# Kernel optimization log

Measured on AMD Instinct MI355X. Metric: run time of the kernel, lower is better.

## Reference

```python
import jax, jax.numpy as jnp
import numpy as np
from jax import lax

B, CIN, COUT, H, W = 4, 256, 256, 64, 64
KH = KW = 3
K = KH * KW
GN_GROUPS = 32
EPS = 1e-5


def setup_inputs() -> dict:
    key = jax.random.key(0)
    ks = jax.random.split(key, 6)
    x = jax.random.normal(ks[0], (B, CIN, H, W), jnp.float32)
    # offset predictor conv: 3x3, 18 out channels, with bias (init small so offsets stay near 0)
    offset_w = jax.random.normal(ks[1], (2 * K, CIN, KH, KW), jnp.float32) * 0.01
    offset_b = jax.random.normal(ks[2], (2 * K,), jnp.float32) * 0.01
    # deformable conv weight (no bias), He-ish scale
    deform_w = jax.random.normal(ks[3], (COUT, CIN, KH, KW), jnp.float32) * (1.0 / np.sqrt(CIN * K))
    gn_gamma = jnp.ones((COUT,), jnp.float32)
    gn_beta = jnp.zeros((COUT,), jnp.float32)
    return {"x": x, "offset_w": offset_w, "offset_b": offset_b,
            "deform_w": deform_w, "gn_gamma": gn_gamma, "gn_beta": gn_beta}


def _deform_conv(x, offset, weight):
    """Deformable conv v1, stride=1, pad=1, dil=1, deformable_groups=1.
    x: [B,C,H,W]; offset: [B,2K,H,W] with (dy,dx) per kernel tap; weight: [O,C,3,3].
    """
    b, c, h, w = x.shape
    off = offset.reshape(b, K, 2, h, w)
    # base sampling grid per kernel tap: p = p0 - pad + k
    ky, kx = jnp.meshgrid(jnp.arange(KH), jnp.arange(KW), indexing="ij")
    base_y = (jnp.arange(h, dtype=jnp.float32) - 1.0)[None, :, None] + ky.reshape(K).astype(jnp.float32)[:, None, None]  # [K,H,1]
    base_x = (jnp.arange(w, dtype=jnp.float32) - 1.0)[None, None, :] + kx.reshape(K).astype(jnp.float32)[:, None, None]  # [K,1,W]
    py = base_y[None] + off[:, :, 0]  # [B,K,H,W]
    px = base_x[None] + off[:, :, 1]  # [B,K,H,W]

    y0 = jnp.floor(py)
    x0 = jnp.floor(px)
    ty = py - y0
    tx = px - x0
    y0 = y0.astype(jnp.int32)
    x0 = x0.astype(jnp.int32)

    x_hw = x.transpose(0, 2, 3, 1).reshape(b, h * w, c)  # [B,HW,C]

    def corner(yi, xi, wgt):
        valid = (yi >= 0) & (yi < h) & (xi >= 0) & (xi < w)
        yc = jnp.clip(yi, 0, h - 1)
        xc = jnp.clip(xi, 0, w - 1)
        idx = (yc * w + xc).reshape(b, K * h * w)
        v = jnp.take_along_axis(x_hw, idx[..., None], axis=1)  # [B,KHW,C]
        return v * (wgt * valid.astype(wgt.dtype)).reshape(b, K * h * w, 1)

    samp = (corner(y0, x0, (1 - ty) * (1 - tx))
            + corner(y0, x0 + 1, (1 - ty) * tx)
            + corner(y0 + 1, x0, ty * (1 - tx))
            + corner(y0 + 1, x0 + 1, ty * tx))  # [B,KHW,C]
    samp = samp.reshape(b, K, h, w, c)
    return jnp.einsum("bkhwc,ock->bohw", samp, weight.reshape(weight.shape[0], c, K))


def reference(x, offset_w, offset_b, deform_w, gn_gamma, gn_beta):
    # offset = conv3x3(x) + bias
    offset = lax.conv_general_dilated(
        x, offset_w, window_strides=(1, 1), padding=((1, 1), (1, 1)),
        dimension_numbers=("NCHW", "OIHW", "NCHW")) + offset_b[None, :, None, None]
    out = _deform_conv(x, offset, deform_w)
    # GroupNorm(32, COUT) + ReLU
    b, c, h, w = out.shape
    g = out.reshape(b, GN_GROUPS, (c // GN_GROUPS) * h * w)
    mu = g.mean(axis=2, keepdims=True)
    var = g.var(axis=2, keepdims=True)
    g = (g - mu) * lax.rsqrt(var + EPS)
    out = g.reshape(b, c, h, w) * gn_gamma[None, :, None, None] + gn_beta[None, :, None, None]
    return jax.nn.relu(out)
```

## Files before the change

kernel.cpp:

```cpp
#include <hip/hip_runtime.h>
#include <hip/hip_bf16.h>
#include <stdint.h>


typedef unsigned short u16;
typedef __bf16 bf16x8 __attribute__((ext_vector_type(8)));
typedef float f32x4_t __attribute__((ext_vector_type(4)));

#define HW 4096

__device__ __forceinline__ uint32_t f32_to_bf16_rne(float f) {
  uint32_t u = __builtin_bit_cast(uint32_t, f);
  return (u + 0x7FFFu + ((u >> 16) & 1u)) >> 16;
}
__device__ __forceinline__ float bf_lo(uint32_t u) {
  return __builtin_bit_cast(float, u << 16);
}
__device__ __forceinline__ float bf_hi(uint32_t u) {
  return __builtin_bit_cast(float, u & 0xFFFF0000u);
}
__device__ __forceinline__ uint32_t blend2(uint32_t a, uint32_t b, uint32_t c,
                                           uint32_t d, float4 mw) {
  float lo = mw.x * bf_lo(a) + mw.y * bf_lo(b) + mw.z * bf_lo(c) + mw.w * bf_lo(d);
  float hi = mw.x * bf_hi(a) + mw.y * bf_hi(b) + mw.z * bf_hi(c) + mw.w * bf_hi(d);
  return f32_to_bf16_rne(lo) | (f32_to_bf16_rne(hi) << 16);
}

__global__ __launch_bounds__(256) void k_transpose(const float* __restrict__ x,
                                                   u16* __restrict__ xt) {
  __shared__ float tile[32][33];
  int b = blockIdx.z;
  int c0 = blockIdx.y * 32;
  int p0 = blockIdx.x * 32;
  int tx = threadIdx.x, ty = threadIdx.y;
#pragma unroll
  for (int j = 0; j < 32; j += 8)
    tile[ty + j][tx] = x[(b * 256 + c0 + ty + j) * HW + p0 + tx];
  __syncthreads();
  int wid = ty * 32 + tx;
  int cp = wid & 15;
  int pr = wid >> 4;
#pragma unroll
  for (int j = 0; j < 2; j++) {
    int p = pr + j * 16;
    uint32_t lo = f32_to_bf16_rne(tile[cp * 2][p]);
    uint32_t hi = f32_to_bf16_rne(tile[cp * 2 + 1][p]);
    *(uint32_t*)&xt[(b * HW + p0 + p) * 256 + c0 + cp * 2] = lo | (hi << 16);
  }
}

__global__ __launch_bounds__(256) void k_prep(const float* __restrict__ wsrc,
                                              const float* __restrict__ ow,
                                              u16* __restrict__ warr,
                                              u16* __restrict__ owm,
                                              float* __restrict__ part) {
  int bid = blockIdx.x;
  if (bid < 2304) {
    int e = bid * 256 + threadIdx.x;
    int kk = e & 7, m = (e >> 3) & 255, g = (e >> 11) & 7, kc = e >> 14;
    int cin = (kc & 3) * 64 + g * 8 + kk;
    int tap = kc >> 2;
    warr[e] = (u16)f32_to_bf16_rne(wsrc[m * 2304 + cin * 9 + tap]);
  } else if (bid < 2592) {
    int e = (bid - 2304) * 256 + threadIdx.x;
    int kk = e & 7, m = (e >> 3) & 31, g = (e >> 8) & 7, kc = e >> 11;
    int cin = (kc & 3) * 64 + g * 8 + kk;
    int tap = kc >> 2;
    float v = (m < 18) ? ow[m * 2304 + cin * 9 + tap] : 0.f;
    owm[e] = (u16)f32_to_bf16_rne(v);
  } else {
    part[threadIdx.x] = 0.f;
  }
}

__global__ __launch_bounds__(512, 4) void k_conv(
    const u16* __restrict__ xt, const u16* __restrict__ warr,
    const u16* __restrict__ owm, const float* __restrict__ ob,
    float* __restrict__ out, float* __restrict__ part) {
  __shared__ char smem[54272];
  u16* stage = (u16*)smem;
  float* off_part = (float*)(smem + 33792);
  int4* ci_s = (int4*)smem;
  float4* mw_s = (float4*)(smem + 4608);
  u16* b_s = (u16*)(smem + 9216);

  int tid = threadIdx.x;
  int lane = tid & 63;
  int wm = tid >> 6;
  int b = blockIdx.x >> 7;
  int pt = blockIdx.x & 127;
  int p0 = pt * 32;
  int yrow = p0 >> 6, xbase = p0 & 63;

  {
    u16* st = stage + wm * 2112;
    int q = lane & 15, pq = lane >> 4;
    int oct = lane & 7, pxs = lane >> 3;
    f32x4_t a2[2][2] = {};
#pragma unroll 1
    for (int kc = wm; kc < 36; kc += 8) {
      int tap = kc >> 2, cc = kc & 3;
      int ky = tap / 3, kx = tap % 3;
      int yy = yrow + ky - 1;
      bool vy = (yy >= 0) && (yy < 64);
#pragma unroll
      for (int i = 0; i < 4; i++) {
        int px = i * 8 + pxs;
        int xx2 = xbase + px + kx - 1;
        uint4 v = make_uint4(0u, 0u, 0u, 0u);
        if (vy && xx2 >= 0 && xx2 < 64)
          v = *(const uint4*)&xt[(b * HW + yy * 64 + xx2) * 256 + cc * 64 + oct * 8];
        *(uint4*)&st[oct * 264 + px * 8] = v;
      }
#pragma unroll
      for (int ks = 0; ks < 2; ks++) {
        int g = ks * 4 + pq;
        const u16* ab = owm + kc * 2048 + g * 256;
#pragma unroll
        for (int s = 0; s < 2; s++) {
          bf16x8 bfr = *(bf16x8*)&st[g * 264 + (s * 16 + q) * 8];
#pragma unroll
          for (int im = 0; im < 2; im++) {
            bf16x8 af = *(const bf16x8*)&ab[(im * 16 + q) * 8];
            a2[s][im] = __builtin_amdgcn_mfma_f32_16x16x32_bf16(af, bfr, a2[s][im], 0, 0, 0);
          }
        }
      }
    }
#pragma unroll
    for (int s = 0; s < 2; s++)
#pragma unroll
      for (int im = 0; im < 2; im++)
#pragma unroll
        for (int r = 0; r < 4; r++) {
          int oc = im * 16 + pq * 4 + r;
          if (oc < 18) off_part[(wm * 32 + s * 16 + q) * 20 + oc] = a2[s][im][r];
        }
  }
  __syncthreads();
  for (int it = tid; it < 288; it += 512) {
    int tap = it >> 5;
    int px = it & 31;
    float dy = ob[2 * tap], dx = ob[2 * tap + 1];
#pragma unroll
    for (int wv = 0; wv < 8; wv++) {
      dy += off_part[(wv * 32 + px) * 20 + 2 * tap];
      dx += off_part[(wv * 32 + px) * 20 + 2 * tap + 1];
    }
    int ky = tap / 3, kx = tap % 3;
    int p = p0 + px;
    int yq = p >> 6, xq = p & 63;
    float py = (float)(yq - 1 + ky) + dy;
    float pxx = (float)(xq - 1 + kx) + dx;
    float y0f = floorf(py), x0f = floorf(pxx);
    float ty = py - y0f, tx = pxx - x0f;
    int y0 = (int)y0f, x0 = (int)x0f;
    int y1 = y0 + 1, x1 = x0 + 1;
    float wy0 = 1.f - ty, wy1 = ty, wx0 = 1.f - tx, wx1 = tx;
    bool vy0 = (y0 >= 0) && (y0 < 64), vy1 = (y1 >= 0) && (y1 < 64);
    bool vx0 = (x0 >= 0) && (x0 < 64), vx1 = (x1 >= 0) && (x1 < 64);
    int cy0 = min(max(y0, 0), 63), cy1 = min(max(y1, 0), 63);
    int cx0 = min(max(x0, 0), 63), cx1 = min(max(x1, 0), 63);
    int base = b * HW;
    int4 ci;
    ci.x = (base + cy0 * 64 + cx0) * 256;
    ci.y = (base + cy0 * 64 + cx1) * 256;
    ci.z = (base + cy1 * 64 + cx0) * 256;
    ci.w = (base + cy1 * 64 + cx1) * 256;
    float4 mw;
    mw.x = wy0 * wx0 * ((vy0 && vx0) ? 1.f : 0.f);
    mw.y = wy0 * wx1 * ((vy0 && vx1) ? 1.f : 0.f);
    mw.z = wy1 * wx0 * ((vy1 && vx0) ? 1.f : 0.f);
    mw.w = wy1 * wx1 * ((vy1 && vx1) ? 1.f : 0.f);
    ci_s[it] = ci;
    mw_s[it] = mw;
  }
  __syncthreads();

  {
    int oct8 = tid & 15;
    int pxg = tid >> 4;
    int sub = pxg >> 4;
    int pxw = pxg & 15;
    int col = lane & 15;
    int pq = lane >> 4;
    f32x4_t acc[2][2] = {};

    int4 ci = ci_s[pxg];
    float4 mw = mw_s[pxg];
    int e = oct8 * 8;
    uint4 c0 = *(const uint4*)&xt[ci.x + e];
    uint4 c1 = *(const uint4*)&xt[ci.y + e];
    uint4 c2 = *(const uint4*)&xt[ci.z + e];
    uint4 c3 = *(const uint4*)&xt[ci.w + e];

#pragma unroll 1
    for (int dccg = 0; dccg < 18; dccg++) {
      u16* bb = b_s + (dccg & 1) * 4352;
      uint4 u;
      u.x = blend2(c0.x, c1.x, c2.x, c3.x, mw);
      u.y = blend2(c0.y, c1.y, c2.y, c3.y, mw);
      u.z = blend2(c0.z, c1.z, c2.z, c3.z, mw);
      u.w = blend2(c0.w, c1.w, c2.w, c3.w, mw);
      *(uint4*)&bb[sub * 2176 + oct8 * 136 + pxw * 8] = u;
      __syncthreads();
      if (dccg < 17) {
        int nx = dccg + 1;
        int tapn = nx >> 1;
        int en = (nx & 1) * 128 + oct8 * 8;
        int4 cin = ci_s[tapn * 32 + pxg];
        float4 mwn = mw_s[tapn * 32 + pxg];
        c0 = *(const uint4*)&xt[cin.x + en];
        c1 = *(const uint4*)&xt[cin.y + en];
        c2 = *(const uint4*)&xt[cin.z + en];
        c3 = *(const uint4*)&xt[cin.w + en];
        mw = mwn;
      }
      int tap = dccg >> 1, dcc = dccg & 1;
#pragma unroll
      for (int ks = 0; ks < 4; ks++) {
        int ro = ks * 4 + pq;
        bf16x8 b0 = *(bf16x8*)&bb[ro * 136 + col * 8];
        bf16x8 b1 = *(bf16x8*)&bb[2176 + ro * 136 + col * 8];
        int kc = tap * 4 + dcc * 2 + (ks >> 1);
        int g = (ks & 1) * 4 + pq;
        const u16* ab = warr + kc * 16384 + g * 2048 + (wm * 32 + col) * 8;
#pragma unroll
        for (int im = 0; im < 2; im++) {
          bf16x8 af = *(const bf16x8*)&ab[im * 128];
          acc[0][im] = __builtin_amdgcn_mfma_f32_16x16x32_bf16(af, b0, acc[0][im], 0, 0, 0);
          acc[1][im] = __builtin_amdgcn_mfma_f32_16x16x32_bf16(af, b1, acc[1][im], 0, 0, 0);
        }
      }
    }

#pragma unroll
    for (int im = 0; im < 2; im++) {
      float s = 0.f, ss = 0.f;
#pragma unroll
      for (int sb = 0; sb < 2; sb++) {
        int n = p0 + sb * 16 + col;
#pragma unroll
        for (int r = 0; r < 4; r++) {
          int m = wm * 32 + im * 16 + pq * 4 + r;
          float v = acc[sb][im][r];
          out[(b * 256 + m) * HW + n] = v;
          s += v;
          ss += v * v;
        }
      }
#pragma unroll
      for (int msk = 1; msk <= 16; msk <<= 1) {
        s += __shfl_xor(s, msk);
        ss += __shfl_xor(ss, msk);
      }
      if ((lane & 31) == 0) {
        int g = wm * 4 + im * 2 + (lane >> 5);
        float* pp = part + (b * 32 + g) * 2;
        atomicAdd(pp, s);
        atomicAdd(pp + 1, ss);
      }
    }
  }
}

__global__ __launch_bounds__(256) void k_gn_apply(float* __restrict__ out,
                                                  const float2* __restrict__ part,
                                                  const float* __restrict__ gamma,
                                                  const float* __restrict__ beta) {
  __shared__ float sga, sbe;
  int gid = blockIdx.x * 256 + threadIdx.x;
  int c = (gid >> 10) & 255;
  int bb = gid >> 18;
  if (threadIdx.x == 0) {
    float2 p = part[bb * 32 + (c >> 3)];
    float mu = p.x / 32768.f;
    float var = p.y / 32768.f - mu * mu;
    float rs = rsqrtf(var + 1e-5f);
    float ga = gamma[c] * rs;
    sga = ga;
    sbe = beta[c] - mu * ga;
  }
  __syncthreads();
  float ga = sga, be = sbe;
  float4 v = ((const float4*)out)[gid];
  v.x = fmaxf(v.x * ga + be, 0.f);
  v.y = fmaxf(v.y * ga + be, 0.f);
  v.z = fmaxf(v.z * ga + be, 0.f);
  v.w = fmaxf(v.w * ga + be, 0.f);
  ((float4*)out)[gid] = v;
}

extern "C" void kernel_launch(void* const* d_in, const int* in_sizes, int n_in,
                              void* d_out, int out_size, void* d_ws, size_t ws_size,
                              hipStream_t stream) {
  const float* x = (const float*)d_in[0];
  const float* offset_w = (const float*)d_in[1];
  const float* offset_b = (const float*)d_in[2];
  const float* deform_w = (const float*)d_in[3];
  const float* gn_gamma = (const float*)d_in[4];
  const float* gn_beta = (const float*)d_in[5];
  float* out = (float*)d_out;
  char* ws = (char*)d_ws;

  u16* xt = (u16*)ws;
  u16* warr = (u16*)(ws + 8388608);
  u16* owm = (u16*)(ws + 9568256);
  float* part = (float*)(ws + 9715712);

  k_transpose<<<dim3(128, 8, 4), dim3(32, 8), 0, stream>>>(x, xt);
  k_prep<<<dim3(2593), dim3(256), 0, stream>>>(deform_w, offset_w, warr, owm, part);
  k_conv<<<dim3(512), dim3(512), 0, stream>>>(xt, warr, owm, offset_b, out, part);
  k_gn_apply<<<dim3(4096), dim3(256), 0, stream>>>(out, (const float2*)part, gn_gamma, gn_beta);
}
```

Measured before the change: 163.4 us.

## Double conv pixel tile to a full row and merge prep kernels

The deformable conv kernel now handles 64 pixels (one full image row) per block instead of 32. That halves the grid to 256 blocks and doubles the MFMA accumulators, so each weight fragment loaded from global memory is reused across twice as many pixels. The offset-prediction phase is split into two halves of 4 waves each, and the block index is swizzled across batch and rows. The transpose and weight-prep kernels are merged into one launch to save a kernel launch. The trade-off is higher register pressure and LDS use, since the occupancy hint was dropped, and fewer blocks on a 256-CU device.

```diff
diff --git a/kernel.cpp b/kernel.cpp
--- a/kernel.cpp
+++ b/kernel.cpp
@@ -26,54 +26,52 @@
   return f32_to_bf16_rne(lo) | (f32_to_bf16_rne(hi) << 16);
 }
 
-__global__ __launch_bounds__(256) void k_transpose(const float* __restrict__ x,
-                                                   u16* __restrict__ xt) {
+__global__ __launch_bounds__(256) void k_pre(const float* __restrict__ x,
+                                             const float* __restrict__ wsrc,
+                                             const float* __restrict__ ow,
+                                             u16* __restrict__ xt,
+                                             u16* __restrict__ warr,
+                                             u16* __restrict__ owm,
+                                             float* __restrict__ part) {
   __shared__ float tile[32][33];
-  int b = blockIdx.z;
-  int c0 = blockIdx.y * 32;
-  int p0 = blockIdx.x * 32;
-  int tx = threadIdx.x, ty = threadIdx.y;
-#pragma unroll
-  for (int j = 0; j < 32; j += 8)
-    tile[ty + j][tx] = x[(b * 256 + c0 + ty + j) * HW + p0 + tx];
-  __syncthreads();
-  int wid = ty * 32 + tx;
-  int cp = wid & 15;
-  int pr = wid >> 4;
-#pragma unroll
-  for (int j = 0; j < 2; j++) {
-    int p = pr + j * 16;
-    uint32_t lo = f32_to_bf16_rne(tile[cp * 2][p]);
-    uint32_t hi = f32_to_bf16_rne(tile[cp * 2 + 1][p]);
-    *(uint32_t*)&xt[(b * HW + p0 + p) * 256 + c0 + cp * 2] = lo | (hi << 16);
-  }
-}
-
-__global__ __launch_bounds__(256) void k_prep(const float* __restrict__ wsrc,
-                                              const float* __restrict__ ow,
-                                              u16* __restrict__ warr,
-                                              u16* __restrict__ owm,
-                                              float* __restrict__ part) {
   int bid = blockIdx.x;
-  if (bid < 2304) {
-    int e = bid * 256 + threadIdx.x;
+  int tid = threadIdx.x;
+  if (bid < 4096) {
+    int bx = bid & 127, by = (bid >> 7) & 7, bz = bid >> 10;
+    int c0 = by * 32, p0 = bx * 32;
+    int tx = tid & 31, ty = tid >> 5;
+#pragma unroll
+    for (int j = 0; j < 32; j += 8)
+      tile[ty + j][tx] = x[(bz * 256 + c0 + ty + j) * HW + p0 + tx];
+    __syncthreads();
+    int cp = tid & 15;
+    int pr = tid >> 4;
+#pragma unroll
+    for (int j = 0; j < 2; j++) {
+      int p = pr + j * 16;
+      uint32_t lo = f32_to_bf16_rne(tile[cp * 2][p]);
+      uint32_t hi = f32_to_bf16_rne(tile[cp * 2 + 1][p]);
+      *(uint32_t*)&xt[(bz * HW + p0 + p) * 256 + c0 + cp * 2] = lo | (hi << 16);
+    }
+  } else if (bid < 6400) {
+    int e = (bid - 4096) * 256 + tid;
     int kk = e & 7, m = (e >> 3) & 255, g = (e >> 11) & 7, kc = e >> 14;
     int cin = (kc & 3) * 64 + g * 8 + kk;
     int tap = kc >> 2;
     warr[e] = (u16)f32_to_bf16_rne(wsrc[m * 2304 + cin * 9 + tap]);
-  } else if (bid < 2592) {
-    int e = (bid - 2304) * 256 + threadIdx.x;
+  } else if (bid < 6688) {
+    int e = (bid - 6400) * 256 + tid;
     int kk = e & 7, m = (e >> 3) & 31, g = (e >> 8) & 7, kc = e >> 11;
     int cin = (kc & 3) * 64 + g * 8 + kk;
     int tap = kc >> 2;
     float v = (m < 18) ? ow[m * 2304 + cin * 9 + tap] : 0.f;
     owm[e] = (u16)f32_to_bf16_rne(v);
   } else {
-    part[threadIdx.x] = 0.f;
-  }
-}
-
-__global__ __launch_bounds__(512, 4) void k_conv(
+    part[tid] = 0.f;
+  }
+}
+
+__global__ __launch_bounds__(512) void k_conv(
     const u16* __restrict__ xt, const u16* __restrict__ warr,
     const u16* __restrict__ owm, const float* __restrict__ ob,
     float* __restrict__ out, float* __restrict__ part) {
@@ -81,32 +79,34 @@
   u16* stage = (u16*)smem;
   float* off_part = (float*)(smem + 33792);
   int4* ci_s = (int4*)smem;
-  float4* mw_s = (float4*)(smem + 4608);
-  u16* b_s = (u16*)(smem + 9216);
+  float4* mw_s = (float4*)(smem + 9216);
+  u16* b_s = (u16*)(smem + 18432);
 
   int tid = threadIdx.x;
   int lane = tid & 63;
   int wm = tid >> 6;
-  int b = blockIdx.x >> 7;
-  int pt = blockIdx.x & 127;
-  int p0 = pt * 32;
-  int yrow = p0 >> 6, xbase = p0 & 63;
+  int wk = (blockIdx.x & 7) * 32 + (blockIdx.x >> 3);
+  int b = wk >> 6;
+  int pt = wk & 63;
+  int p0 = pt * 64;
 
   {
     u16* st = stage + wm * 2112;
+    int half = wm >> 2, ww = wm & 3;
+    int xh = half * 32;
     int q = lane & 15, pq = lane >> 4;
     int oct = lane & 7, pxs = lane >> 3;
     f32x4_t a2[2][2] = {};
 #pragma unroll 1
-    for (int kc = wm; kc < 36; kc += 8) {
+    for (int kc = ww; kc < 36; kc += 4) {
       int tap = kc >> 2, cc = kc & 3;
       int ky = tap / 3, kx = tap % 3;
-      int yy = yrow + ky - 1;
+      int yy = pt + ky - 1;
       bool vy = (yy >= 0) && (yy < 64);
 #pragma unroll
       for (int i = 0; i < 4; i++) {
         int px = i * 8 + pxs;
-        int xx2 = xbase + px + kx - 1;
+        int xx2 = xh + px + kx - 1;
         uint4 v = make_uint4(0u, 0u, 0u, 0u);
         if (vy && xx2 >= 0 && xx2 < 64)
           v = *(const uint4*)&xt[(b * HW + yy * 64 + xx2) * 256 + cc * 64 + oct * 8];
@@ -138,20 +138,19 @@
         }
   }
   __syncthreads();
-  for (int it = tid; it < 288; it += 512) {
-    int tap = it >> 5;
-    int px = it & 31;
+  for (int it = tid; it < 576; it += 512) {
+    int tap = it >> 6;
+    int px = it & 63;
+    int half = px >> 5, px32 = px & 31;
     float dy = ob[2 * tap], dx = ob[2 * tap + 1];
 #pragma unroll
-    for (int wv = 0; wv < 8; wv++) {
-      dy += off_part[(wv * 32 + px) * 20 + 2 * tap];
-      dx += off_part[(wv * 32 + px) * 20 + 2 * tap + 1];
+    for (int wv = 0; wv < 4; wv++) {
+      dy += off_part[((half * 4 + wv) * 32 + px32) * 20 + 2 * tap];
+      dx += off_part[((half * 4 + wv) * 32 + px32) * 20 + 2 * tap + 1];
     }
     int ky = tap / 3, kx = tap % 3;
-    int p = p0 + px;
-    int yq = p >> 6, xq = p & 63;
-    float py = (float)(yq - 1 + ky) + dy;
-    float pxx = (float)(xq - 1 + kx) + dx;
+    float py = (float)(pt - 1 + ky) + dy;
+    float pxx = (float)(px - 1 + kx) + dx;
     float y0f = floorf(py), x0f = floorf(pxx);
     float ty = py - y0f, tx = pxx - x0f;
     int y0 = (int)y0f, x0 = (int)x0f;
@@ -180,41 +179,62 @@
   {
     int oct8 = tid & 15;
     int pxg = tid >> 4;
-    int sub = pxg >> 4;
+    int suba = pxg >> 4;
     int pxw = pxg & 15;
     int col = lane & 15;
     int pq = lane >> 4;
-    f32x4_t acc[2][2] = {};
-
-    int4 ci = ci_s[pxg];
-    float4 mw = mw_s[pxg];
-    int e = oct8 * 8;
-    uint4 c0 = *(const uint4*)&xt[ci.x + e];
-    uint4 c1 = *(const uint4*)&xt[ci.y + e];
-    uint4 c2 = *(const uint4*)&xt[ci.z + e];
-    uint4 c3 = *(const uint4*)&xt[ci.w + e];
+    f32x4_t acc[4][2] = {};
+
+    int e0 = oct8 * 8;
+    int4 cia = ci_s[pxg];
+    float4 mwa = mw_s[pxg];
+    int4 cib = ci_s[32 + pxg];
+    float4 mwb = mw_s[32 + pxg];
+    uint4 g0 = *(const uint4*)&xt[cia.x + e0];
+    uint4 g1 = *(const uint4*)&xt[cia.y + e0];
+    uint4 g2 = *(const uint4*)&xt[cia.z + e0];
+    uint4 g3 = *(const uint4*)&xt[cia.w + e0];
+    uint4 h0 = *(const uint4*)&xt[cib.x + e0];
+    uint4 h1 = *(const uint4*)&xt[cib.y + e0];
+    uint4 h2 = *(const uint4*)&xt[cib.z + e0];
+    uint4 h3 = *(const uint4*)&xt[cib.w + e0];
 
 #pragma unroll 1
     for (int dccg = 0; dccg < 18; dccg++) {
-      u16* bb = b_s + (dccg & 1) * 4352;
-      uint4 u;
-      u.x = blend2(c0.x, c1.x, c2.x, c3.x, mw);
-      u.y = blend2(c0.y, c1.y, c2.y, c3.y, mw);
-      u.z = blend2(c0.z, c1.z, c2.z, c3.z, mw);
-      u.w = blend2(c0.w, c1.w, c2.w, c3.w, mw);
-      *(uint4*)&bb[sub * 2176 + oct8 * 136 + pxw * 8] = u;
+      u16* bb = b_s + (dccg & 1) * 8704;
+      {
+        uint4 u;
+        u.x = blend2(g0.x, g1.x, g2.x, g3.x, mwa);
+        u.y = blend2(g0.y, g1.y, g2.y, g3.y, mwa);
+        u.z = blend2(g0.z, g1.z, g2.z, g3.z, mwa);
+        u.w = blend2(g0.w, g1.w, g2.w, g3.w, mwa);
+        *(uint4*)&bb[suba * 2176 + oct8 * 136 + pxw * 8] = u;
+      }
+      {
+        uint4 u;
+        u.x = blend2(h0.x, h1.x, h2.x, h3.x, mwb);
+        u.y = blend2(h0.y, h1.y, h2.y, h3.y, mwb);
+        u.z = blend2(h0.z, h1.z, h2.z, h3.z, mwb);
+        u.w = blend2(h0.w, h1.w, h2.w, h3.w, mwb);
+        *(uint4*)&bb[(suba + 2) * 2176 + oct8 * 136 + pxw * 8] = u;
+      }
       __syncthreads();
       if (dccg < 17) {
         int nx = dccg + 1;
         int tapn = nx >> 1;
-        int en = (nx & 1) * 128 + oct8 * 8;
-        int4 cin = ci_s[tapn * 32 + pxg];
-        float4 mwn = mw_s[tapn * 32 + pxg];
-        c0 = *(const uint4*)&xt[cin.x + en];
-        c1 = *(const uint4*)&xt[cin.y + en];
-        c2 = *(const uint4*)&xt[cin.z + en];
-        c3 = *(const uint4*)&xt[cin.w + en];
-        mw = mwn;
+        int en = (nx & 1) * 128 + e0;
+        cia = ci_s[tapn * 64 + pxg];
+        mwa = mw_s[tapn * 64 + pxg];
+        cib = ci_s[tapn * 64 + 32 + pxg];
+        mwb = mw_s[tapn * 64 + 32 + pxg];
+        g0 = *(const uint4*)&xt[cia.x + en];
+        g1 = *(const uint4*)&xt[cia.y + en];
+        g2 = *(const uint4*)&xt[cia.z + en];
+        g3 = *(const uint4*)&xt[cia.w + en];
+        h0 = *(const uint4*)&xt[cib.x + en];
+        h1 = *(const uint4*)&xt[cib.y + en];
+        h2 = *(const uint4*)&xt[cib.z + en];
+        h3 = *(const uint4*)&xt[cib.w + en];
       }
       int tap = dccg >> 1, dcc = dccg & 1;
 #pragma unroll
@@ -222,14 +242,18 @@
         int ro = ks * 4 + pq;
         bf16x8 b0 = *(bf16x8*)&bb[ro * 136 + col * 8];
         bf16x8 b1 = *(bf16x8*)&bb[2176 + ro * 136 + col * 8];
+        bf16x8 b2 = *(bf16x8*)&bb[4352 + ro * 136 + col * 8];
+        bf16x8 b3 = *(bf16x8*)&bb[6528 + ro * 136 + col * 8];
         int kc = tap * 4 + dcc * 2 + (ks >> 1);
-        int g = (ks & 1) * 4 + pq;
-        const u16* ab = warr + kc * 16384 + g * 2048 + (wm * 32 + col) * 8;
+        int gg = (ks & 1) * 4 + pq;
+        const u16* ab = warr + kc * 16384 + gg * 2048 + (wm * 32 + col) * 8;
 #pragma unroll
         for (int im = 0; im < 2; im++) {
           bf16x8 af = *(const bf16x8*)&ab[im * 128];
           acc[0][im] = __builtin_amdgcn_mfma_f32_16x16x32_bf16(af, b0, acc[0][im], 0, 0, 0);
           acc[1][im] = __builtin_amdgcn_mfma_f32_16x16x32_bf16(af, b1, acc[1][im], 0, 0, 0);
+          acc[2][im] = __builtin_amdgcn_mfma_f32_16x16x32_bf16(af, b2, acc[2][im], 0, 0, 0);
+          acc[3][im] = __builtin_amdgcn_mfma_f32_16x16x32_bf16(af, b3, acc[3][im], 0, 0, 0);
         }
       }
     }
@@ -238,7 +262,7 @@
     for (int im = 0; im < 2; im++) {
       float s = 0.f, ss = 0.f;
 #pragma unroll
-      for (int sb = 0; sb < 2; sb++) {
+      for (int sb = 0; sb < 4; sb++) {
         int n = p0 + sb * 16 + col;
 #pragma unroll
         for (int r = 0; r < 4; r++) {
@@ -255,8 +279,8 @@
         ss += __shfl_xor(ss, msk);
       }
       if ((lane & 31) == 0) {
-        int g = wm * 4 + im * 2 + (lane >> 5);
-        float* pp = part + (b * 32 + g) * 2;
+        int grp = wm * 4 + im * 2 + (lane >> 5);
+        float* pp = part + (b * 32 + grp) * 2;
         atomicAdd(pp, s);
         atomicAdd(pp + 1, ss);
       }
@@ -308,8 +332,7 @@
   u16* owm = (u16*)(ws + 9568256);
   float* part = (float*)(ws + 9715712);
 
-  k_transpose<<<dim3(128, 8, 4), dim3(32, 8), 0, stream>>>(x, xt);
-  k_prep<<<dim3(2593), dim3(256), 0, stream>>>(deform_w, offset_w, warr, owm, part);
-  k_conv<<<dim3(512), dim3(512), 0, stream>>>(xt, warr, owm, offset_b, out, part);
+  k_pre<<<dim3(6689), dim3(256), 0, stream>>>(x, deform_w, offset_w, xt, warr, owm, part);
+  k_conv<<<dim3(256), dim3(512), 0, stream>>>(xt, warr, owm, offset_b, out, part);
   k_gn_apply<<<dim3(4096), dim3(256), 0, stream>>>(out, (const float2*)part, gn_gamma, gn_beta);
 }
```

Measured after the change: 173.9 us. 1.06x slower.

## Merge prep kernels and gather deformable samples directly into MFMA registers

Applied to the files above, without the earlier changes.

Fuses the transpose and weight-prep kernels into one launch. The deformable conv drops from 8 to 4 waves per block, each wave now covering 64 output channels. Each lane gathers and bilinearly blends its own B-fragment straight into registers, removing the shared-memory staging buffer and its per-step __syncthreads. Blocks are remapped across batch/tile in an interleaved order, and the offset conv loop is restructured to process taps per wave. This trades barrier and LDS traffic for redundant global gathers across waves and higher register pressure.

```diff
diff --git a/kernel.cpp b/kernel.cpp
--- a/kernel.cpp
+++ b/kernel.cpp
@@ -26,103 +26,103 @@
   return f32_to_bf16_rne(lo) | (f32_to_bf16_rne(hi) << 16);
 }
 
-__global__ __launch_bounds__(256) void k_transpose(const float* __restrict__ x,
-                                                   u16* __restrict__ xt) {
+__global__ __launch_bounds__(256) void k_pre(const float* __restrict__ x,
+                                             const float* __restrict__ wsrc,
+                                             const float* __restrict__ ow,
+                                             u16* __restrict__ xt,
+                                             u16* __restrict__ warr,
+                                             u16* __restrict__ owm,
+                                             float* __restrict__ part) {
   __shared__ float tile[32][33];
-  int b = blockIdx.z;
-  int c0 = blockIdx.y * 32;
-  int p0 = blockIdx.x * 32;
-  int tx = threadIdx.x, ty = threadIdx.y;
-#pragma unroll
-  for (int j = 0; j < 32; j += 8)
-    tile[ty + j][tx] = x[(b * 256 + c0 + ty + j) * HW + p0 + tx];
-  __syncthreads();
-  int wid = ty * 32 + tx;
-  int cp = wid & 15;
-  int pr = wid >> 4;
-#pragma unroll
-  for (int j = 0; j < 2; j++) {
-    int p = pr + j * 16;
-    uint32_t lo = f32_to_bf16_rne(tile[cp * 2][p]);
-    uint32_t hi = f32_to_bf16_rne(tile[cp * 2 + 1][p]);
-    *(uint32_t*)&xt[(b * HW + p0 + p) * 256 + c0 + cp * 2] = lo | (hi << 16);
-  }
-}
-
-__global__ __launch_bounds__(256) void k_prep(const float* __restrict__ wsrc,
-                                              const float* __restrict__ ow,
-                                              u16* __restrict__ warr,
-                                              u16* __restrict__ owm,
-                                              float* __restrict__ part) {
   int bid = blockIdx.x;
-  if (bid < 2304) {
-    int e = bid * 256 + threadIdx.x;
+  int tid = threadIdx.x;
+  if (bid < 4096) {
+    int bx = bid & 127, by = (bid >> 7) & 7, bz = bid >> 10;
+    int c0 = by * 32, p0 = bx * 32;
+    int tx = tid & 31, ty = tid >> 5;
+#pragma unroll
+    for (int j = 0; j < 32; j += 8)
+      tile[ty + j][tx] = x[(bz * 256 + c0 + ty + j) * HW + p0 + tx];
+    __syncthreads();
+    int cp = tid & 15;
+    int pr = tid >> 4;
+#pragma unroll
+    for (int j = 0; j < 2; j++) {
+      int p = pr + j * 16;
+      uint32_t lo = f32_to_bf16_rne(tile[cp * 2][p]);
+      uint32_t hi = f32_to_bf16_rne(tile[cp * 2 + 1][p]);
+      *(uint32_t*)&xt[(bz * HW + p0 + p) * 256 + c0 + cp * 2] = lo | (hi << 16);
+    }
+  } else if (bid < 6400) {
+    int e = (bid - 4096) * 256 + tid;
     int kk = e & 7, m = (e >> 3) & 255, g = (e >> 11) & 7, kc = e >> 14;
     int cin = (kc & 3) * 64 + g * 8 + kk;
     int tap = kc >> 2;
     warr[e] = (u16)f32_to_bf16_rne(wsrc[m * 2304 + cin * 9 + tap]);
-  } else if (bid < 2592) {
-    int e = (bid - 2304) * 256 + threadIdx.x;
+  } else if (bid < 6688) {
+    int e = (bid - 6400) * 256 + tid;
     int kk = e & 7, m = (e >> 3) & 31, g = (e >> 8) & 7, kc = e >> 11;
     int cin = (kc & 3) * 64 + g * 8 + kk;
     int tap = kc >> 2;
     float v = (m < 18) ? ow[m * 2304 + cin * 9 + tap] : 0.f;
     owm[e] = (u16)f32_to_bf16_rne(v);
   } else {
-    part[threadIdx.x] = 0.f;
-  }
-}
-
-__global__ __launch_bounds__(512, 4) void k_conv(
+    part[tid] = 0.f;
+  }
+}
+
+__global__ __launch_bounds__(256, 2) void k_conv(
     const u16* __restrict__ xt, const u16* __restrict__ warr,
     const u16* __restrict__ owm, const float* __restrict__ ob,
     float* __restrict__ out, float* __restrict__ part) {
-  __shared__ char smem[54272];
+  __shared__ char smem[27136];
   u16* stage = (u16*)smem;
-  float* off_part = (float*)(smem + 33792);
+  float* off_part = (float*)(smem + 16896);
   int4* ci_s = (int4*)smem;
   float4* mw_s = (float4*)(smem + 4608);
-  u16* b_s = (u16*)(smem + 9216);
 
   int tid = threadIdx.x;
   int lane = tid & 63;
   int wm = tid >> 6;
-  int b = blockIdx.x >> 7;
-  int pt = blockIdx.x & 127;
+  int wk = (blockIdx.x & 7) * 64 + (blockIdx.x >> 3);
+  int b = wk >> 7;
+  int pt = wk & 127;
   int p0 = pt * 32;
   int yrow = p0 >> 6, xbase = p0 & 63;
 
   {
     u16* st = stage + wm * 2112;
     int q = lane & 15, pq = lane >> 4;
-    int oct = lane & 7, pxs = lane >> 3;
     f32x4_t a2[2][2] = {};
 #pragma unroll 1
-    for (int kc = wm; kc < 36; kc += 8) {
-      int tap = kc >> 2, cc = kc & 3;
+    for (int tap = wm; tap < 9; tap += 4) {
       int ky = tap / 3, kx = tap % 3;
       int yy = yrow + ky - 1;
       bool vy = (yy >= 0) && (yy < 64);
 #pragma unroll
-      for (int i = 0; i < 4; i++) {
-        int px = i * 8 + pxs;
-        int xx2 = xbase + px + kx - 1;
-        uint4 v = make_uint4(0u, 0u, 0u, 0u);
-        if (vy && xx2 >= 0 && xx2 < 64)
-          v = *(const uint4*)&xt[(b * HW + yy * 64 + xx2) * 256 + cc * 64 + oct * 8];
-        *(uint4*)&st[oct * 264 + px * 8] = v;
-      }
-#pragma unroll
-      for (int ks = 0; ks < 2; ks++) {
-        int g = ks * 4 + pq;
-        const u16* ab = owm + kc * 2048 + g * 256;
-#pragma unroll
-        for (int s = 0; s < 2; s++) {
-          bf16x8 bfr = *(bf16x8*)&st[g * 264 + (s * 16 + q) * 8];
-#pragma unroll
-          for (int im = 0; im < 2; im++) {
-            bf16x8 af = *(const bf16x8*)&ab[(im * 16 + q) * 8];
-            a2[s][im] = __builtin_amdgcn_mfma_f32_16x16x32_bf16(af, bfr, a2[s][im], 0, 0, 0);
+      for (int cc = 0; cc < 4; cc++) {
+        int kc = tap * 4 + cc;
+#pragma unroll
+        for (int i = 0; i < 8; i++) {
+          int px = i * 4 + pq;
+          int xx2 = xbase + px + kx - 1;
+          uint2 v = make_uint2(0u, 0u);
+          if (vy && xx2 >= 0 && xx2 < 64)
+            v = *(const uint2*)&xt[(b * HW + yy * 64 + xx2) * 256 + cc * 64 + q * 4];
+          *(uint2*)&st[(q >> 1) * 264 + px * 8 + (q & 1) * 4] = v;
+        }
+#pragma unroll
+        for (int ks = 0; ks < 2; ks++) {
+          int g = ks * 4 + pq;
+          const u16* ab = owm + kc * 2048 + g * 256;
+#pragma unroll
+          for (int s = 0; s < 2; s++) {
+            bf16x8 bfr = *(bf16x8*)&st[g * 264 + (s * 16 + q) * 8];
+#pragma unroll
+            for (int im = 0; im < 2; im++) {
+              bf16x8 af = *(const bf16x8*)&ab[(im * 16 + q) * 8];
+              a2[s][im] = __builtin_amdgcn_mfma_f32_16x16x32_bf16(af, bfr, a2[s][im], 0, 0, 0);
+            }
           }
         }
       }
@@ -138,12 +138,12 @@
         }
   }
   __syncthreads();
-  for (int it = tid; it < 288; it += 512) {
+  for (int it = tid; it < 288; it += 256) {
     int tap = it >> 5;
     int px = it & 31;
     float dy = ob[2 * tap], dx = ob[2 * tap + 1];
 #pragma unroll
-    for (int wv = 0; wv < 8; wv++) {
+    for (int wv = 0; wv < 4; wv++) {
       dy += off_part[(wv * 32 + px) * 20 + 2 * tap];
       dx += off_part[(wv * 32 + px) * 20 + 2 * tap + 1];
     }
@@ -178,71 +178,62 @@
   __syncthreads();
 
   {
-    int oct8 = tid & 15;
-    int pxg = tid >> 4;
-    int sub = pxg >> 4;
-    int pxw = pxg & 15;
     int col = lane & 15;
     int pq = lane >> 4;
-    f32x4_t acc[2][2] = {};
-
-    int4 ci = ci_s[pxg];
-    float4 mw = mw_s[pxg];
-    int e = oct8 * 8;
-    uint4 c0 = *(const uint4*)&xt[ci.x + e];
-    uint4 c1 = *(const uint4*)&xt[ci.y + e];
-    uint4 c2 = *(const uint4*)&xt[ci.z + e];
-    uint4 c3 = *(const uint4*)&xt[ci.w + e];
+    f32x4_t acc[2][4] = {};
 
 #pragma unroll 1
-    for (int dccg = 0; dccg < 18; dccg++) {
-      u16* bb = b_s + (dccg & 1) * 4352;
-      uint4 u;
-      u.x = blend2(c0.x, c1.x, c2.x, c3.x, mw);
-      u.y = blend2(c0.y, c1.y, c2.y, c3.y, mw);
-      u.z = blend2(c0.z, c1.z, c2.z, c3.z, mw);
-      u.w = blend2(c0.w, c1.w, c2.w, c3.w, mw);
-      *(uint4*)&bb[sub * 2176 + oct8 * 136 + pxw * 8] = u;
-      __syncthreads();
-      if (dccg < 17) {
-        int nx = dccg + 1;
-        int tapn = nx >> 1;
-        int en = (nx & 1) * 128 + oct8 * 8;
-        int4 cin = ci_s[tapn * 32 + pxg];
-        float4 mwn = mw_s[tapn * 32 + pxg];
-        c0 = *(const uint4*)&xt[cin.x + en];
-        c1 = *(const uint4*)&xt[cin.y + en];
-        c2 = *(const uint4*)&xt[cin.z + en];
-        c3 = *(const uint4*)&xt[cin.w + en];
-        mw = mwn;
-      }
-      int tap = dccg >> 1, dcc = dccg & 1;
-#pragma unroll
-      for (int ks = 0; ks < 4; ks++) {
-        int ro = ks * 4 + pq;
-        bf16x8 b0 = *(bf16x8*)&bb[ro * 136 + col * 8];
-        bf16x8 b1 = *(bf16x8*)&bb[2176 + ro * 136 + col * 8];
-        int kc = tap * 4 + dcc * 2 + (ks >> 1);
-        int g = (ks & 1) * 4 + pq;
-        const u16* ab = warr + kc * 16384 + g * 2048 + (wm * 32 + col) * 8;
-#pragma unroll
-        for (int im = 0; im < 2; im++) {
-          bf16x8 af = *(const bf16x8*)&ab[im * 128];
-          acc[0][im] = __builtin_amdgcn_mfma_f32_16x16x32_bf16(af, b0, acc[0][im], 0, 0, 0);
-          acc[1][im] = __builtin_amdgcn_mfma_f32_16x16x32_bf16(af, b1, acc[1][im], 0, 0, 0);
-        }
-      }
-    }
-
-#pragma unroll
-    for (int im = 0; im < 2; im++) {
+    for (int tap = 0; tap < 9; tap++) {
+      int4 ci0 = ci_s[tap * 32 + col];
+      int4 ci1 = ci_s[tap * 32 + 16 + col];
+      float4 mw0 = mw_s[tap * 32 + col];
+      float4 mw1 = mw_s[tap * 32 + 16 + col];
+#pragma unroll 2
+      for (int cc = 0; cc < 4; cc++) {
+        int kc = tap * 4 + cc;
+        const u16* wbase = warr + kc * 16384 + pq * 2048 + (wm * 64 + col) * 8;
+#pragma unroll
+        for (int h = 0; h < 2; h++) {
+          int e = cc * 64 + h * 32 + pq * 8;
+          uint4 a0 = *(const uint4*)&xt[ci0.x + e];
+          uint4 a1 = *(const uint4*)&xt[ci0.y + e];
+          uint4 a2v = *(const uint4*)&xt[ci0.z + e];
+          uint4 a3 = *(const uint4*)&xt[ci0.w + e];
+          uint4 b0 = *(const uint4*)&xt[ci1.x + e];
+          uint4 b1 = *(const uint4*)&xt[ci1.y + e];
+          uint4 b2 = *(const uint4*)&xt[ci1.z + e];
+          uint4 b3 = *(const uint4*)&xt[ci1.w + e];
+          uint4 f0, f1;
+          f0.x = blend2(a0.x, a1.x, a2v.x, a3.x, mw0);
+          f0.y = blend2(a0.y, a1.y, a2v.y, a3.y, mw0);
+          f0.z = blend2(a0.z, a1.z, a2v.z, a3.z, mw0);
+          f0.w = blend2(a0.w, a1.w, a2v.w, a3.w, mw0);
+          f1.x = blend2(b0.x, b1.x, b2.x, b3.x, mw1);
+          f1.y = blend2(b0.y, b1.y, b2.y, b3.y, mw1);
+          f1.z = blend2(b0.z, b1.z, b2.z, b3.z, mw1);
+          f1.w = blend2(b0.w, b1.w, b2.w, b3.w, mw1);
+          bf16x8 bf0 = *(bf16x8*)&f0;
+          bf16x8 bf1 = *(bf16x8*)&f1;
+          const u16* ab = wbase + h * 4 * 2048;
+#pragma unroll
+          for (int im = 0; im < 4; im++) {
+            bf16x8 af = *(const bf16x8*)&ab[im * 128];
+            acc[0][im] = __builtin_amdgcn_mfma_f32_16x16x32_bf16(af, bf0, acc[0][im], 0, 0, 0);
+            acc[1][im] = __builtin_amdgcn_mfma_f32_16x16x32_bf16(af, bf1, acc[1][im], 0, 0, 0);
+          }
+        }
+      }
+    }
+
+#pragma unroll
+    for (int im = 0; im < 4; im++) {
       float s = 0.f, ss = 0.f;
 #pragma unroll
       for (int sb = 0; sb < 2; sb++) {
         int n = p0 + sb * 16 + col;
 #pragma unroll
         for (int r = 0; r < 4; r++) {
-          int m = wm * 32 + im * 16 + pq * 4 + r;
+          int m = wm * 64 + im * 16 + pq * 4 + r;
           float v = acc[sb][im][r];
           out[(b * 256 + m) * HW + n] = v;
           s += v;
@@ -255,8 +246,8 @@
         ss += __shfl_xor(ss, msk);
       }
       if ((lane & 31) == 0) {
-        int g = wm * 4 + im * 2 + (lane >> 5);
-        float* pp = part + (b * 32 + g) * 2;
+        int grp = wm * 8 + im * 2 + (lane >> 5);
+        float* pp = part + (b * 32 + grp) * 2;
         atomicAdd(pp, s);
         atomicAdd(pp + 1, ss);
       }
@@ -308,8 +299,7 @@
   u16* owm = (u16*)(ws + 9568256);
   float* part = (float*)(ws + 9715712);
 
-  k_transpose<<<dim3(128, 8, 4), dim3(32, 8), 0, stream>>>(x, xt);
-  k_prep<<<dim3(2593), dim3(256), 0, stream>>>(deform_w, offset_w, warr, owm, part);
-  k_conv<<<dim3(512), dim3(512), 0, stream>>>(xt, warr, owm, offset_b, out, part);
+  k_pre<<<dim3(6689), dim3(256), 0, stream>>>(x, deform_w, offset_w, xt, warr, owm, part);
+  k_conv<<<dim3(512), dim3(256), 0, stream>>>(xt, warr, owm, offset_b, out, part);
   k_gn_apply<<<dim3(4096), dim3(256), 0, stream>>>(out, (const float2*)part, gn_gamma, gn_beta);
 }
```

Result: slower. 268.1 us (+64.1%).

## Split deformable conv into offset/sampling kernel and GEMM kernel via workspace buffer

Applied to the files above, without the earlier changes.

Merges the transpose and weight-prep kernels into one launch. The fused conv kernel is split in two: one kernel predicts offsets and writes bilinearly sampled bf16 columns to a large workspace matrix, and a separate MFMA kernel reads that matrix with double-buffered LDS and computes the output plus GroupNorm partial sums. Block indices are swizzled across batches. The aim is better occupancy and overlap in each phase, at the cost of roughly 75 MB of extra global write and read traffic. The old fused kernel is kept as a fallback when the workspace is too small.

```diff
diff --git a/kernel.cpp b/kernel.cpp
--- a/kernel.cpp
+++ b/kernel.cpp
@@ -26,103 +26,102 @@
   return f32_to_bf16_rne(lo) | (f32_to_bf16_rne(hi) << 16);
 }
 
-__global__ __launch_bounds__(256) void k_transpose(const float* __restrict__ x,
-                                                   u16* __restrict__ xt) {
+__global__ __launch_bounds__(256) void k_pre(const float* __restrict__ x,
+                                             const float* __restrict__ wsrc,
+                                             const float* __restrict__ ow,
+                                             u16* __restrict__ xt,
+                                             u16* __restrict__ warr,
+                                             u16* __restrict__ owm,
+                                             float* __restrict__ part) {
   __shared__ float tile[32][33];
-  int b = blockIdx.z;
-  int c0 = blockIdx.y * 32;
-  int p0 = blockIdx.x * 32;
-  int tx = threadIdx.x, ty = threadIdx.y;
-#pragma unroll
-  for (int j = 0; j < 32; j += 8)
-    tile[ty + j][tx] = x[(b * 256 + c0 + ty + j) * HW + p0 + tx];
-  __syncthreads();
-  int wid = ty * 32 + tx;
-  int cp = wid & 15;
-  int pr = wid >> 4;
-#pragma unroll
-  for (int j = 0; j < 2; j++) {
-    int p = pr + j * 16;
-    uint32_t lo = f32_to_bf16_rne(tile[cp * 2][p]);
-    uint32_t hi = f32_to_bf16_rne(tile[cp * 2 + 1][p]);
-    *(uint32_t*)&xt[(b * HW + p0 + p) * 256 + c0 + cp * 2] = lo | (hi << 16);
-  }
-}
-
-__global__ __launch_bounds__(256) void k_prep(const float* __restrict__ wsrc,
-                                              const float* __restrict__ ow,
-                                              u16* __restrict__ warr,
-                                              u16* __restrict__ owm,
-                                              float* __restrict__ part) {
   int bid = blockIdx.x;
-  if (bid < 2304) {
-    int e = bid * 256 + threadIdx.x;
+  int tid = threadIdx.x;
+  if (bid < 4096) {
+    int bx = bid & 127, by = (bid >> 7) & 7, bz = bid >> 10;
+    int c0 = by * 32, p0 = bx * 32;
+    int tx = tid & 31, ty = tid >> 5;
+#pragma unroll
+    for (int j = 0; j < 32; j += 8)
+      tile[ty + j][tx] = x[(bz * 256 + c0 + ty + j) * HW + p0 + tx];
+    __syncthreads();
+    int cp = tid & 15;
+    int pr = tid >> 4;
+#pragma unroll
+    for (int j = 0; j < 2; j++) {
+      int p = pr + j * 16;
+      uint32_t lo = f32_to_bf16_rne(tile[cp * 2][p]);
+      uint32_t hi = f32_to_bf16_rne(tile[cp * 2 + 1][p]);
+      *(uint32_t*)&xt[(bz * HW + p0 + p) * 256 + c0 + cp * 2] = lo | (hi << 16);
+    }
+  } else if (bid < 6400) {
+    int e = (bid - 4096) * 256 + tid;
     int kk = e & 7, m = (e >> 3) & 255, g = (e >> 11) & 7, kc = e >> 14;
     int cin = (kc & 3) * 64 + g * 8 + kk;
     int tap = kc >> 2;
     warr[e] = (u16)f32_to_bf16_rne(wsrc[m * 2304 + cin * 9 + tap]);
-  } else if (bid < 2592) {
-    int e = (bid - 2304) * 256 + threadIdx.x;
+  } else if (bid < 6688) {
+    int e = (bid - 6400) * 256 + tid;
     int kk = e & 7, m = (e >> 3) & 31, g = (e >> 8) & 7, kc = e >> 11;
     int cin = (kc & 3) * 64 + g * 8 + kk;
     int tap = kc >> 2;
     float v = (m < 18) ? ow[m * 2304 + cin * 9 + tap] : 0.f;
     owm[e] = (u16)f32_to_bf16_rne(v);
   } else {
-    part[threadIdx.x] = 0.f;
-  }
-}
-
-__global__ __launch_bounds__(512, 4) void k_conv(
-    const u16* __restrict__ xt, const u16* __restrict__ warr,
-    const u16* __restrict__ owm, const float* __restrict__ ob,
-    float* __restrict__ out, float* __restrict__ part) {
-  __shared__ char smem[54272];
+    part[tid] = 0.f;
+  }
+}
+
+__global__ __launch_bounds__(256, 2) void k_off(
+    const u16* __restrict__ xt, const u16* __restrict__ owm,
+    const float* __restrict__ ob, u16* __restrict__ bmat) {
+  __shared__ char smem[27136];
   u16* stage = (u16*)smem;
-  float* off_part = (float*)(smem + 33792);
+  float* off_part = (float*)(smem + 16896);
   int4* ci_s = (int4*)smem;
   float4* mw_s = (float4*)(smem + 4608);
-  u16* b_s = (u16*)(smem + 9216);
 
   int tid = threadIdx.x;
   int lane = tid & 63;
   int wm = tid >> 6;
-  int b = blockIdx.x >> 7;
-  int pt = blockIdx.x & 127;
+  int wk = (blockIdx.x & 7) * 64 + (blockIdx.x >> 3);
+  int b = wk >> 7;
+  int pt = wk & 127;
   int p0 = pt * 32;
   int yrow = p0 >> 6, xbase = p0 & 63;
 
   {
     u16* st = stage + wm * 2112;
     int q = lane & 15, pq = lane >> 4;
-    int oct = lane & 7, pxs = lane >> 3;
     f32x4_t a2[2][2] = {};
 #pragma unroll 1
-    for (int kc = wm; kc < 36; kc += 8) {
-      int tap = kc >> 2, cc = kc & 3;
+    for (int tap = wm; tap < 9; tap += 4) {
       int ky = tap / 3, kx = tap % 3;
       int yy = yrow + ky - 1;
       bool vy = (yy >= 0) && (yy < 64);
 #pragma unroll
-      for (int i = 0; i < 4; i++) {
-        int px = i * 8 + pxs;
-        int xx2 = xbase + px + kx - 1;
-        uint4 v = make_uint4(0u, 0u, 0u, 0u);
-        if (vy && xx2 >= 0 && xx2 < 64)
-          v = *(const uint4*)&xt[(b * HW + yy * 64 + xx2) * 256 + cc * 64 + oct * 8];
-        *(uint4*)&st[oct * 264 + px * 8] = v;
-      }
-#pragma unroll
-      for (int ks = 0; ks < 2; ks++) {
-        int g = ks * 4 + pq;
-        const u16* ab = owm + kc * 2048 + g * 256;
-#pragma unroll
-        for (int s = 0; s < 2; s++) {
-          bf16x8 bfr = *(bf16x8*)&st[g * 264 + (s * 16 + q) * 8];
-#pragma unroll
-          for (int im = 0; im < 2; im++) {
-            bf16x8 af = *(const bf16x8*)&ab[(im * 16 + q) * 8];
-            a2[s][im] = __builtin_amdgcn_mfma_f32_16x16x32_bf16(af, bfr, a2[s][im], 0, 0, 0);
+      for (int cc = 0; cc < 4; cc++) {
+        int kc = tap * 4 + cc;
+#pragma unroll
+        for (int i = 0; i < 8; i++) {
+          int px = i * 4 + pq;
+          int xx2 = xbase + px + kx - 1;
+          uint2 v = make_uint2(0u, 0u);
+          if (vy && xx2 >= 0 && xx2 < 64)
+            v = *(const uint2*)&xt[(b * HW + yy * 64 + xx2) * 256 + cc * 64 + q * 4];
+          *(uint2*)&st[(q >> 1) * 264 + px * 8 + (q & 1) * 4] = v;
+        }
+#pragma unroll
+        for (int ks = 0; ks < 2; ks++) {
+          int g = ks * 4 + pq;
+          const u16* ab = owm + kc * 2048 + g * 256;
+#pragma unroll
+          for (int s = 0; s < 2; s++) {
+            bf16x8 bfr = *(bf16x8*)&st[g * 264 + (s * 16 + q) * 8];
+#pragma unroll
+            for (int im = 0; im < 2; im++) {
+              bf16x8 af = *(const bf16x8*)&ab[(im * 16 + q) * 8];
+              a2[s][im] = __builtin_amdgcn_mfma_f32_16x16x32_bf16(af, bfr, a2[s][im], 0, 0, 0);
+            }
           }
         }
       }
@@ -138,12 +137,12 @@
         }
   }
   __syncthreads();
-  for (int it = tid; it < 288; it += 512) {
+  for (int it = tid; it < 288; it += 256) {
     int tap = it >> 5;
     int px = it & 31;
     float dy = ob[2 * tap], dx = ob[2 * tap + 1];
 #pragma unroll
-    for (int wv = 0; wv < 8; wv++) {
+    for (int wv = 0; wv < 4; wv++) {
       dy += off_part[(wv * 32 + px) * 20 + 2 * tap];
       dx += off_part[(wv * 32 + px) * 20 + 2 * tap + 1];
     }
@@ -177,6 +176,205 @@
   }
   __syncthreads();
 
+  u16* bt = bmat + (size_t)wk * 73728;
+#pragma unroll 1
+  for (int it = 0; it < 36; it++) {
+    int idx = it * 256 + tid;
+    int oct = idx & 31;
+    int px = (idx >> 5) & 31;
+    int tap = idx >> 10;
+    int4 ci = ci_s[tap * 32 + px];
+    float4 mw = mw_s[tap * 32 + px];
+    int e = oct * 8;
+    uint4 c0 = *(const uint4*)&xt[ci.x + e];
+    uint4 c1 = *(const uint4*)&xt[ci.y + e];
+    uint4 c2 = *(const uint4*)&xt[ci.z + e];
+    uint4 c3 = *(const uint4*)&xt[ci.w + e];
+    uint4 u;
+    u.x = blend2(c0.x, c1.x, c2.x, c3.x, mw);
+    u.y = blend2(c0.y, c1.y, c2.y, c3.y, mw);
+    u.z = blend2(c0.z, c1.z, c2.z, c3.z, mw);
+    u.w = blend2(c0.w, c1.w, c2.w, c3.w, mw);
+    *(uint4*)&bt[((tap * 32 + oct) * 32 + px) * 8] = u;
+  }
+}
+
+__global__ __launch_bounds__(512, 8) void k_mm(
+    const u16* __restrict__ warr, const u16* __restrict__ bmat,
+    float* __restrict__ out, float* __restrict__ part) {
+  __shared__ u16 b_s[8192];
+
+  int tid = threadIdx.x;
+  int lane = tid & 63;
+  int wm = tid >> 6;
+  int wk = (blockIdx.x & 7) * 64 + (blockIdx.x >> 3);
+  int b = wk >> 7;
+  int pt = wk & 127;
+  int p0 = pt * 32;
+  int col = lane & 15;
+  int pq = lane >> 4;
+  const u16* bt = bmat + (size_t)wk * 73728;
+
+  f32x4_t acc[2][2] = {};
+  uint4 cur = *(const uint4*)&bt[tid * 8];
+
+#pragma unroll 1
+  for (int d = 0; d < 18; d++) {
+    u16* bb = b_s + (d & 1) * 4096;
+    *(uint4*)&bb[tid * 8] = cur;
+    __syncthreads();
+    if (d < 17) cur = *(const uint4*)&bt[(d + 1) * 4096 + tid * 8];
+    int tap = d >> 1, half = d & 1;
+#pragma unroll
+    for (int ks = 0; ks < 4; ks++) {
+      int ro = ks * 4 + pq;
+      bf16x8 b0 = *(bf16x8*)&bb[(ro * 32 + col) * 8];
+      bf16x8 b1 = *(bf16x8*)&bb[(ro * 32 + 16 + col) * 8];
+      int kc = tap * 4 + half * 2 + (ks >> 1);
+      int gg = (ks & 1) * 4 + pq;
+      const u16* ab = warr + kc * 16384 + gg * 2048 + (wm * 32 + col) * 8;
+#pragma unroll
+      for (int im = 0; im < 2; im++) {
+        bf16x8 af = *(const bf16x8*)&ab[im * 128];
+        acc[0][im] = __builtin_amdgcn_mfma_f32_16x16x32_bf16(af, b0, acc[0][im], 0, 0, 0);
+        acc[1][im] = __builtin_amdgcn_mfma_f32_16x16x32_bf16(af, b1, acc[1][im], 0, 0, 0);
+      }
+    }
+  }
+
+#pragma unroll
+  for (int im = 0; im < 2; im++) {
+    float s = 0.f, ss = 0.f;
+#pragma unroll
+    for (int sb = 0; sb < 2; sb++) {
+      int n = p0 + sb * 16 + col;
+#pragma unroll
+      for (int r = 0; r < 4; r++) {
+        int m = wm * 32 + im * 16 + pq * 4 + r;
+        float v = acc[sb][im][r];
+        out[(b * 256 + m) * HW + n] = v;
+        s += v;
+        ss += v * v;
+      }
+    }
+#pragma unroll
+    for (int msk = 1; msk <= 16; msk <<= 1) {
+      s += __shfl_xor(s, msk);
+      ss += __shfl_xor(ss, msk);
+    }
+    if ((lane & 31) == 0) {
+      int grp = wm * 4 + im * 2 + (lane >> 5);
+      float* pp = part + (b * 32 + grp) * 2;
+      atomicAdd(pp, s);
+      atomicAdd(pp + 1, ss);
+    }
+  }
+}
+
+__global__ __launch_bounds__(512, 4) void k_conv(
+    const u16* __restrict__ xt, const u16* __restrict__ warr,
+    const u16* __restrict__ owm, const float* __restrict__ ob,
+    float* __restrict__ out, float* __restrict__ part) {
+  __shared__ char smem[54272];
+  u16* stage = (u16*)smem;
+  float* off_part = (float*)(smem + 33792);
+  int4* ci_s = (int4*)smem;
+  float4* mw_s = (float4*)(smem + 4608);
+  u16* b_s = (u16*)(smem + 9216);
+
+  int tid = threadIdx.x;
+  int lane = tid & 63;
+  int wm = tid >> 6;
+  int b = blockIdx.x >> 7;
+  int pt = blockIdx.x & 127;
+  int p0 = pt * 32;
+  int yrow = p0 >> 6, xbase = p0 & 63;
+
+  {
+    u16* st = stage + wm * 2112;
+    int q = lane & 15, pq = lane >> 4;
+    int oct = lane & 7, pxs = lane >> 3;
+    f32x4_t a2[2][2] = {};
+#pragma unroll 1
+    for (int kc = wm; kc < 36; kc += 8) {
+      int tap = kc >> 2, cc = kc & 3;
+      int ky = tap / 3, kx = tap % 3;
+      int yy = yrow + ky - 1;
+      bool vy = (yy >= 0) && (yy < 64);
+#pragma unroll
+      for (int i = 0; i < 4; i++) {
+        int px = i * 8 + pxs;
+        int xx2 = xbase + px + kx - 1;
+        uint4 v = make_uint4(0u, 0u, 0u, 0u);
+        if (vy && xx2 >= 0 && xx2 < 64)
+          v = *(const uint4*)&xt[(b * HW + yy * 64 + xx2) * 256 + cc * 64 + oct * 8];
+        *(uint4*)&st[oct * 264 + px * 8] = v;
+      }
+#pragma unroll
+      for (int ks = 0; ks < 2; ks++) {
+        int g = ks * 4 + pq;
+        const u16* ab = owm + kc * 2048 + g * 256;
+#pragma unroll
+        for (int s = 0; s < 2; s++) {
+          bf16x8 bfr = *(bf16x8*)&st[g * 264 + (s * 16 + q) * 8];
+#pragma unroll
+          for (int im = 0; im < 2; im++) {
+            bf16x8 af = *(const bf16x8*)&ab[(im * 16 + q) * 8];
+            a2[s][im] = __builtin_amdgcn_mfma_f32_16x16x32_bf16(af, bfr, a2[s][im], 0, 0, 0);
+          }
+        }
+      }
+    }
+#pragma unroll
+    for (int s = 0; s < 2; s++)
+#pragma unroll
+      for (int im = 0; im < 2; im++)
+#pragma unroll
+        for (int r = 0; r < 4; r++) {
+          int oc = im * 16 + pq * 4 + r;
+          if (oc < 18) off_part[(wm * 32 + s * 16 + q) * 20 + oc] = a2[s][im][r];
+        }
+  }
+  __syncthreads();
+  for (int it = tid; it < 288; it += 512) {
+    int tap = it >> 5;
+    int px = it & 31;
+    float dy = ob[2 * tap], dx = ob[2 * tap + 1];
+#pragma unroll
+    for (int wv = 0; wv < 8; wv++) {
+      dy += off_part[(wv * 32 + px) * 20 + 2 * tap];
+      dx += off_part[(wv * 32 + px) * 20 + 2 * tap + 1];
+    }
+    int ky = tap / 3, kx = tap % 3;
+    int p = p0 + px;
+    int yq = p >> 6, xq = p & 63;
+    float py = (float)(yq - 1 + ky) + dy;
+    float pxx = (float)(xq - 1 + kx) + dx;
+    float y0f = floorf(py), x0f = floorf(pxx);
+    float ty = py - y0f, tx = pxx - x0f;
+    int y0 = (int)y0f, x0 = (int)x0f;
+    int y1 = y0 + 1, x1 = x0 + 1;
+    float wy0 = 1.f - ty, wy1 = ty, wx0 = 1.f - tx, wx1 = tx;
+    bool vy0 = (y0 >= 0) && (y0 < 64), vy1 = (y1 >= 0) && (y1 < 64);
+    bool vx0 = (x0 >= 0) && (x0 < 64), vx1 = (x1 >= 0) && (x1 < 64);
+    int cy0 = min(max(y0, 0), 63), cy1 = min(max(y1, 0), 63);
+    int cx0 = min(max(x0, 0), 63), cx1 = min(max(x1, 0), 63);
+    int base = b * HW;
+    int4 ci;
+    ci.x = (base + cy0 * 64 + cx0) * 256;
+    ci.y = (base + cy0 * 64 + cx1) * 256;
+    ci.z = (base + cy1 * 64 + cx0) * 256;
+    ci.w = (base + cy1 * 64 + cx1) * 256;
+    float4 mw;
+    mw.x = wy0 * wx0 * ((vy0 && vx0) ? 1.f : 0.f);
+    mw.y = wy0 * wx1 * ((vy0 && vx1) ? 1.f : 0.f);
+    mw.z = wy1 * wx0 * ((vy1 && vx0) ? 1.f : 0.f);
+    mw.w = wy1 * wx1 * ((vy1 && vx1) ? 1.f : 0.f);
+    ci_s[it] = ci;
+    mw_s[it] = mw;
+  }
+  __syncthreads();
+
   {
     int oct8 = tid & 15;
     int pxg = tid >> 4;
@@ -307,9 +505,14 @@
   u16* warr = (u16*)(ws + 8388608);
   u16* owm = (u16*)(ws + 9568256);
   float* part = (float*)(ws + 9715712);
-
-  k_transpose<<<dim3(128, 8, 4), dim3(32, 8), 0, stream>>>(x, xt);
-  k_prep<<<dim3(2593), dim3(256), 0, stream>>>(deform_w, offset_w, warr, owm, part);
-  k_conv<<<dim3(512), dim3(512), 0, stream>>>(xt, warr, owm, offset_b, out, part);
+  u16* bmat = (u16*)(ws + 9716736);
+
+  k_pre<<<dim3(6689), dim3(256), 0, stream>>>(x, deform_w, offset_w, xt, warr, owm, part);
+  if (ws_size >= 85214208ull) {
+    k_off<<<dim3(512), dim3(256), 0, stream>>>(xt, owm, offset_b, bmat);
+    k_mm<<<dim3(512), dim3(512), 0, stream>>>(warr, bmat, out, part);
+  } else {
+    k_conv<<<dim3(512), dim3(512), 0, stream>>>(xt, warr, owm, offset_b, out, part);
+  }
   k_gn_apply<<<dim3(4096), dim3(256), 0, stream>>>(out, (const float2*)part, gn_gamma, gn_beta);
 }
```

Result: slower. 184.1 us (+12.7%).
